# Optimization experiments

Hardware: AMD Instinct MI355X
Metric: run time of the kernel (lower is better)

The kernel has to match this reference:

```python
import jax, jax.numpy as jnp
import numpy as np

NBINS = 256  # skimage threshold_otsu default


def _otsu_threshold(x):
    """Global Otsu threshold over the whole array, matching skimage.filters.threshold_otsu."""
    counts, edges = jnp.histogram(x.reshape(-1), bins=NBINS)
    counts = counts.astype(jnp.float32)
    centers = 0.5 * (edges[:-1] + edges[1:])  # [NBINS]

    # class probabilities / weights for all candidate thresholds
    w1 = jnp.cumsum(counts)                       # weight of class <= t
    w2 = jnp.cumsum(counts[::-1])[::-1]           # weight of class > t
    csum = jnp.cumsum(counts * centers)
    csum_rev = jnp.cumsum((counts * centers)[::-1])[::-1]
    m1 = csum / jnp.maximum(w1, 1.0)              # class means (guard empty bins)
    m2 = csum_rev / jnp.maximum(w2, 1.0)

    # between-class variance at each split point
    var12 = w1[:-1] * w2[1:] * (m1[:-1] - m2[1:]) ** 2  # [NBINS-1]
    idx = jnp.argmax(var12)
    return centers[idx]


def setup_inputs() -> dict:
    key = jax.random.key(0)
    inputs = jax.random.normal(key, (16, 1024, 2048, 1), dtype=jnp.float32)
    return {"inputs": inputs}


def reference(inputs) -> jnp.ndarray:
    x = inputs.astype(jnp.float32)
    thresh = _otsu_threshold(x)
    # ((image > thresh) * 1).astype(float32)
    return (x > thresh).astype(jnp.float32)
```

## Files before the change

### kernel.cpp

```cpp
#include <hip/hip_runtime.h>
#include <stdint.h>

#define NBINS 256
#define NCOPY 32
#define GRID 2048
#define TPB 256
#define HOFF 4
#define MOFF 512
#define XOFF (512 + GRID)
#define PKOFF 8192

typedef float f32x4 __attribute__((ext_vector_type(4)));

__device__ __forceinline__ float edge_at(int i, float minv, float delta) {
    return __fadd_rn(__fmul_rn((float)i, delta), minv);
}
__device__ __forceinline__ float min4(float4 v) {
    return fminf(fminf(v.x, v.y), fminf(v.z, v.w));
}
__device__ __forceinline__ float max4(float4 v) {
    return fmaxf(fmaxf(v.x, v.y), fmaxf(v.z, v.w));
}

__global__ void __launch_bounds__(TPB) k_minmax(const float* __restrict__ in,
                                                int n, uint32_t* ws) {
    float* fws = (float*)ws;
    int n4 = n >> 2;
    int chunk = (n4 + GRID - 1) / GRID;
    int start = blockIdx.x * chunk;
    int end = start + chunk; if (end > n4) end = n4;
    const float4* in4 = (const float4*)in;
    float vmin = INFINITY, vmax = -INFINITY;

    int i = start + threadIdx.x;
    for (; i + 7 * TPB < end; i += 8 * TPB) {
        float4 v0 = in4[i];
        float4 v1 = in4[i + TPB];
        float4 v2 = in4[i + 2 * TPB];
        float4 v3 = in4[i + 3 * TPB];
        float4 v4 = in4[i + 4 * TPB];
        float4 v5 = in4[i + 5 * TPB];
        float4 v6 = in4[i + 6 * TPB];
        float4 v7 = in4[i + 7 * TPB];
        float mn0 = fminf(fminf(min4(v0), min4(v1)), fminf(min4(v2), min4(v3)));
        float mn1 = fminf(fminf(min4(v4), min4(v5)), fminf(min4(v6), min4(v7)));
        float mx0 = fmaxf(fmaxf(max4(v0), max4(v1)), fmaxf(max4(v2), max4(v3)));
        float mx1 = fmaxf(fmaxf(max4(v4), max4(v5)), fmaxf(max4(v6), max4(v7)));
        vmin = fminf(vmin, fminf(mn0, mn1));
        vmax = fmaxf(vmax, fmaxf(mx0, mx1));
    }
    for (; i < end; i += TPB) {
        float4 v = in4[i];
        vmin = fminf(vmin, min4(v));
        vmax = fmaxf(vmax, max4(v));
    }
    for (int j = (n4 << 2) + blockIdx.x * TPB + threadIdx.x; j < n; j += GRID * TPB) {
        float v = in[j];
        vmin = fminf(vmin, v);
        vmax = fmaxf(vmax, v);
    }
#pragma unroll
    for (int off = 32; off > 0; off >>= 1) {
        vmin = fminf(vmin, __shfl_down(vmin, off));
        vmax = fmaxf(vmax, __shfl_down(vmax, off));
    }
    __shared__ float smin[4], smax[4];
    int wave = threadIdx.x >> 6, lane = threadIdx.x & 63;
    if (lane == 0) { smin[wave] = vmin; smax[wave] = vmax; }
    __syncthreads();
    if (threadIdx.x == 0) {
        fws[MOFF + blockIdx.x] = fminf(fminf(smin[0], smin[1]), fminf(smin[2], smin[3]));
        fws[XOFF + blockIdx.x] = fmaxf(fmaxf(smax[0], smax[1]), fmaxf(smax[2], smax[3]));
    }
    if (blockIdx.x == 0) ws[HOFF + threadIdx.x] = 0;
}

__device__ __forceinline__ int bin_of(float v, float minv, float invd) {
    float t = (v - minv) * invd;
    t = fminf(fmaxf(t, 0.0f), 255.0f);
    return (int)t;
}

__device__ __forceinline__ uint32_t binbit(float v, float minv, float invd,
                                           float delta, uint32_t* bit) {
    int j = bin_of(v, minv, invd);
    float e0 = edge_at(j, minv, delta);
    float e1 = edge_at(j + 1, minv, delta);
    float ctr = __fmul_rn(0.5f, __fadd_rn(e0, e1));
    *bit = (v > ctr) ? 1u : 0u;
    return (uint32_t)j;
}

__global__ void __launch_bounds__(TPB) k_hist(const float* __restrict__ in,
                                              int n, uint32_t* ws, int packed) {
    __shared__ uint32_t h[NBINS * NCOPY];
    float* hf = (float*)h;
    float* fws = (float*)ws;

    float lmin = INFINITY, lmax = -INFINITY;
    for (int k = threadIdx.x; k < GRID; k += TPB) {
        lmin = fminf(lmin, fws[MOFF + k]);
        lmax = fmaxf(lmax, fws[XOFF + k]);
    }
#pragma unroll
    for (int off = 32; off > 0; off >>= 1) {
        lmin = fminf(lmin, __shfl_down(lmin, off));
        lmax = fmaxf(lmax, __shfl_down(lmax, off));
    }
    int wave = threadIdx.x >> 6, lane = threadIdx.x & 63;
    if (lane == 0) { hf[wave] = lmin; hf[8 + wave] = lmax; }
    __syncthreads();
    float minv = fminf(fminf(hf[0], hf[1]), fminf(hf[2], hf[3]));
    float maxv = fmaxf(fmaxf(hf[8], hf[9]), fmaxf(hf[10], hf[11]));
    float invd = __fdiv_rn(256.0f, __fsub_rn(maxv, minv));
    float delta = __fdiv_rn(__fsub_rn(maxv, minv), 256.0f);
    __syncthreads();
    for (int i = threadIdx.x; i < NBINS * NCOPY; i += TPB) h[i] = 0;
    __syncthreads();

    int c = threadIdx.x & (NCOPY - 1);
    int n4 = n >> 2;
    int chunk = (n4 + GRID - 1) / GRID;
    int start = blockIdx.x * chunk;
    int end = start + chunk; if (end > n4) end = n4;
    const float4* in4 = (const float4*)in;
    uint32_t* bins = ws + PKOFF;
    uint8_t* bits8 = (uint8_t*)(ws + PKOFF + n4);

    for (int i = start + threadIdx.x; i < end; i += TPB) {
        float4 q = in4[i];
        uint32_t b0, b1, b2, b3;
        uint32_t j0 = binbit(q.x, minv, invd, delta, &b0);
        uint32_t j1 = binbit(q.y, minv, invd, delta, &b1);
        uint32_t j2 = binbit(q.z, minv, invd, delta, &b2);
        uint32_t j3 = binbit(q.w, minv, invd, delta, &b3);
        atomicAdd(&h[j0 * NCOPY + c], 1u);
        atomicAdd(&h[j1 * NCOPY + c], 1u);
        atomicAdd(&h[j2 * NCOPY + c], 1u);
        atomicAdd(&h[j3 * NCOPY + c], 1u);
        if (packed) {
            bins[i] = j0 | (j1 << 8) | (j2 << 16) | (j3 << 24);
            bits8[i] = (uint8_t)(b0 | (b1 << 1) | (b2 << 2) | (b3 << 3));
        }
    }
    for (int j = (n4 << 2) + blockIdx.x * TPB + threadIdx.x; j < n; j += GRID * TPB) {
        atomicAdd(&h[bin_of(in[j], minv, invd) * NCOPY + c], 1u);
    }
    __syncthreads();
    for (int b = threadIdx.x; b < NBINS; b += TPB) {
        uint32_t s = 0;
#pragma unroll
        for (int k = 0; k < NCOPY; ++k) s += h[b * NCOPY + k];
        if (s) atomicAdd(&ws[HOFF + b], s);
    }
}

__device__ __forceinline__ void otsu_prologue(const uint32_t* __restrict__ ws,
                                              int* best_out, float* thresh_out) {
    __shared__ float cnt[NBINS], ctr[NBINS], w1[NBINS], w2[NBINS],
                     cs[NBINS], csr[NBINS], scan[NBINS];
    __shared__ int sbest;
    const float* fws = (const float*)ws;
    int i = threadIdx.x;

    float lmin = INFINITY, lmax = -INFINITY;
    for (int k = i; k < GRID; k += TPB) {
        lmin = fminf(lmin, fws[MOFF + k]);
        lmax = fmaxf(lmax, fws[XOFF + k]);
    }
#pragma unroll
    for (int off = 32; off > 0; off >>= 1) {
        lmin = fminf(lmin, __shfl_down(lmin, off));
        lmax = fmaxf(lmax, __shfl_down(lmax, off));
    }
    int wave = i >> 6, lane = i & 63;
    if (lane == 0) { scan[wave] = lmin; scan[8 + wave] = lmax; }
    __syncthreads();
    float minv = fminf(fminf(scan[0], scan[1]), fminf(scan[2], scan[3]));
    float maxv = fmaxf(fmaxf(scan[8], scan[9]), fmaxf(scan[10], scan[11]));
    float delta = __fdiv_rn(__fsub_rn(maxv, minv), 256.0f);
    __syncthreads();

    cnt[i] = (float)ws[HOFF + i];
    float e0 = edge_at(i, minv, delta);
    float e1 = edge_at(i + 1, minv, delta);
    ctr[i] = __fmul_rn(0.5f, __fadd_rn(e0, e1));
    __syncthreads();

    scan[i] = cnt[i]; __syncthreads();
    for (int off = 1; off < NBINS; off <<= 1) {
        float v = scan[i];
        if (i >= off) v = __fadd_rn(scan[i - off], v);
        __syncthreads(); scan[i] = v; __syncthreads();
    }
    w1[i] = scan[i]; __syncthreads();

    scan[i] = __fmul_rn(cnt[i], ctr[i]); __syncthreads();
    for (int off = 1; off < NBINS; off <<= 1) {
        float v = scan[i];
        if (i >= off) v = __fadd_rn(scan[i - off], v);
        __syncthreads(); scan[i] = v; __syncthreads();
    }
    cs[i] = scan[i]; __syncthreads();

    scan[i] = cnt[i]; __syncthreads();
    for (int off = 1; off < NBINS; off <<= 1) {
        float v = scan[i];
        if (i + off < NBINS) v = __fadd_rn(v, scan[i + off]);
        __syncthreads(); scan[i] = v; __syncthreads();
    }
    w2[i] = scan[i]; __syncthreads();

    scan[i] = __fmul_rn(cnt[i], ctr[i]); __syncthreads();
    for (int off = 1; off < NBINS; off <<= 1) {
        float v = scan[i];
        if (i + off < NBINS) v = __fadd_rn(v, scan[i + off]);
        __syncthreads(); scan[i] = v; __syncthreads();
    }
    csr[i] = scan[i]; __syncthreads();

    if (i < NBINS - 1) {
        float m1 = __fdiv_rn(cs[i], fmaxf(w1[i], 1.0f));
        float m2 = __fdiv_rn(csr[i + 1], fmaxf(w2[i + 1], 1.0f));
        float d = __fsub_rn(m1, m2);
        scan[i] = __fmul_rn(__fmul_rn(w1[i], w2[i + 1]), __fmul_rn(d, d));
    }
    __syncthreads();
    if (i == 0) {
        int best = 0; float bv = scan[0];
        for (int k = 1; k < NBINS - 1; ++k) {
            float v = scan[k];
            if (v > bv) { bv = v; best = k; }
        }
        sbest = best;
        scan[0] = ctr[best];
    }
    __syncthreads();
    *best_out = sbest;
    *thresh_out = scan[0];
    __syncthreads();
}

__device__ __forceinline__ f32x4 verdict4(uint32_t u, uint32_t bt, uint32_t ubest) {
    f32x4 r;
    uint32_t j0 = u & 255u, j1 = (u >> 8) & 255u,
             j2 = (u >> 16) & 255u, j3 = (u >> 24) & 255u;
    r.x = (j0 > ubest || (j0 == ubest && (bt & 1u))) ? 1.0f : 0.0f;
    r.y = (j1 > ubest || (j1 == ubest && (bt & 2u))) ? 1.0f : 0.0f;
    r.z = (j2 > ubest || (j2 == ubest && (bt & 4u))) ? 1.0f : 0.0f;
    r.w = (j3 > ubest || (j3 == ubest && (bt & 8u))) ? 1.0f : 0.0f;
    return r;
}

__global__ void __launch_bounds__(TPB) k_bin_packed(const float* __restrict__ in,
                                                    float* __restrict__ out,
                                                    int n,
                                                    const uint32_t* __restrict__ ws) {
    int best; float t;
    otsu_prologue(ws, &best, &t);

    int n4 = n >> 2;
    int chunk = (n4 + GRID - 1) / GRID;
    int start = blockIdx.x * chunk;
    int end = start + chunk; if (end > n4) end = n4;
    const uint32_t* bins = ws + PKOFF;
    const uint8_t* bits8 = (const uint8_t*)(ws + PKOFF + n4);
    f32x4* out4 = (f32x4*)out;
    uint32_t ubest = (uint32_t)best;

    for (int i = start + threadIdx.x; i < end; i += TPB) {
        f32x4 r = verdict4(bins[i], bits8[i], ubest);
        __builtin_nontemporal_store(r, &out4[i]);
    }
    for (int j = (n4 << 2) + blockIdx.x * TPB + threadIdx.x; j < n; j += GRID * TPB) {
        float r = in[j] > t ? 1.0f : 0.0f;
        __builtin_nontemporal_store(r, &out[j]);
    }
}

__global__ void __launch_bounds__(TPB) k_bin_direct(const float* __restrict__ in,
                                                    float* __restrict__ out,
                                                    int n,
                                                    const uint32_t* __restrict__ ws) {
    int best; float t;
    otsu_prologue(ws, &best, &t);

    int n4 = n >> 2;
    int chunk = (n4 + GRID - 1) / GRID;
    int start = blockIdx.x * chunk;
    int end = start + chunk; if (end > n4) end = n4;
    const float4* in4 = (const float4*)in;
    float4* out4 = (float4*)out;
    int i = start + threadIdx.x;
    for (; i + 3 * TPB < end; i += 4 * TPB) {
        float4 v0 = in4[i];
        float4 v1 = in4[i + TPB];
        float4 v2 = in4[i + 2 * TPB];
        float4 v3 = in4[i + 3 * TPB];
        float4 r0, r1, r2, r3;
        r0.x = v0.x > t ? 1.0f : 0.0f; r0.y = v0.y > t ? 1.0f : 0.0f;
        r0.z = v0.z > t ? 1.0f : 0.0f; r0.w = v0.w > t ? 1.0f : 0.0f;
        r1.x = v1.x > t ? 1.0f : 0.0f; r1.y = v1.y > t ? 1.0f : 0.0f;
        r1.z = v1.z > t ? 1.0f : 0.0f; r1.w = v1.w > t ? 1.0f : 0.0f;
        r2.x = v2.x > t ? 1.0f : 0.0f; r2.y = v2.y > t ? 1.0f : 0.0f;
        r2.z = v2.z > t ? 1.0f : 0.0f; r2.w = v2.w > t ? 1.0f : 0.0f;
        r3.x = v3.x > t ? 1.0f : 0.0f; r3.y = v3.y > t ? 1.0f : 0.0f;
        r3.z = v3.z > t ? 1.0f : 0.0f; r3.w = v3.w > t ? 1.0f : 0.0f;
        out4[i] = r0;
        out4[i + TPB] = r1;
        out4[i + 2 * TPB] = r2;
        out4[i + 3 * TPB] = r3;
    }
    for (; i < end; i += TPB) {
        float4 v = in4[i];
        float4 r;
        r.x = v.x > t ? 1.0f : 0.0f;
        r.y = v.y > t ? 1.0f : 0.0f;
        r.z = v.z > t ? 1.0f : 0.0f;
        r.w = v.w > t ? 1.0f : 0.0f;
        out4[i] = r;
    }
    for (int j = (n4 << 2) + blockIdx.x * TPB + threadIdx.x; j < n; j += GRID * TPB) {
        out[j] = in[j] > t ? 1.0f : 0.0f;
    }
}

extern "C" void kernel_launch(void* const* d_in, const int* in_sizes, int n_in,
                              void* d_out, int out_size, void* d_ws, size_t ws_size,
                              hipStream_t stream) {
    const float* in = (const float*)d_in[0];
    float* out = (float*)d_out;
    uint32_t* ws = (uint32_t*)d_ws;
    int n = in_sizes[0];
    int n4 = n >> 2;

    size_t need = (size_t)(PKOFF + (size_t)n4) * 4 + (size_t)n4;
    int packed = (ws_size >= need) ? 1 : 0;

    hipLaunchKernelGGL(k_minmax, dim3(GRID), dim3(TPB), 0, stream, in, n, ws);
    hipLaunchKernelGGL(k_hist, dim3(GRID), dim3(TPB), 0, stream, in, n, ws, packed);
    if (packed) {
        hipLaunchKernelGGL(k_bin_packed, dim3(GRID), dim3(TPB), 0, stream,
                           in, out, n, ws);
    } else {
        hipLaunchKernelGGL(k_bin_direct, dim3(GRID), dim3(TPB), 0, stream,
                           in, out, n, ws);
    }
}
```

Before: 142.2 us.

## Compute Otsu threshold once in last histogram block via atomic ticket

Moves the Otsu scan/argmax out of every block of the binarize kernels and into the histogram kernel: the last block to finish (detected with an atomic ticket counter) computes the best bin and threshold and publishes them to workspace. The binarize kernels then just read two words instead of each of 2048 blocks re-reducing min/max and running four serial shared-memory scans. The histogram kernel gains a fence and atomic per block, and the tail block does the serial work. It reuses the histogram shared buffer for scan storage and relies on minv/delta already being available there.

```diff
diff --git a/kernel.cpp b/kernel.cpp
--- a/kernel.cpp
+++ b/kernel.cpp
@@ -5,6 +5,9 @@
 #define NCOPY 32
 #define GRID 2048
 #define TPB 256
+#define BEST 1
+#define THRS 2
+#define TICK 3
 #define HOFF 4
 #define MOFF 512
 #define XOFF (512 + GRID)
@@ -72,7 +75,10 @@
         fws[MOFF + blockIdx.x] = fminf(fminf(smin[0], smin[1]), fminf(smin[2], smin[3]));
         fws[XOFF + blockIdx.x] = fmaxf(fmaxf(smax[0], smax[1]), fmaxf(smax[2], smax[3]));
     }
-    if (blockIdx.x == 0) ws[HOFF + threadIdx.x] = 0;
+    if (blockIdx.x == 0) {
+        ws[HOFF + threadIdx.x] = 0;
+        if (threadIdx.x == 0) { ws[BEST] = 0; ws[THRS] = 0; ws[TICK] = 0; }
+    }
 }
 
 __device__ __forceinline__ int bin_of(float v, float minv, float invd) {
@@ -153,92 +159,87 @@
         for (int k = 0; k < NCOPY; ++k) s += h[b * NCOPY + k];
         if (s) atomicAdd(&ws[HOFF + b], s);
     }
-}
-
-__device__ __forceinline__ void otsu_prologue(const uint32_t* __restrict__ ws,
-                                              int* best_out, float* thresh_out) {
-    __shared__ float cnt[NBINS], ctr[NBINS], w1[NBINS], w2[NBINS],
-                     cs[NBINS], csr[NBINS], scan[NBINS];
-    __shared__ int sbest;
-    const float* fws = (const float*)ws;
-    int i = threadIdx.x;
-
-    float lmin = INFINITY, lmax = -INFINITY;
-    for (int k = i; k < GRID; k += TPB) {
-        lmin = fminf(lmin, fws[MOFF + k]);
-        lmax = fmaxf(lmax, fws[XOFF + k]);
-    }
-#pragma unroll
-    for (int off = 32; off > 0; off >>= 1) {
-        lmin = fminf(lmin, __shfl_down(lmin, off));
-        lmax = fmaxf(lmax, __shfl_down(lmax, off));
-    }
-    int wave = i >> 6, lane = i & 63;
-    if (lane == 0) { scan[wave] = lmin; scan[8 + wave] = lmax; }
-    __syncthreads();
-    float minv = fminf(fminf(scan[0], scan[1]), fminf(scan[2], scan[3]));
-    float maxv = fmaxf(fmaxf(scan[8], scan[9]), fmaxf(scan[10], scan[11]));
-    float delta = __fdiv_rn(__fsub_rn(maxv, minv), 256.0f);
-    __syncthreads();
-
-    cnt[i] = (float)ws[HOFF + i];
-    float e0 = edge_at(i, minv, delta);
-    float e1 = edge_at(i + 1, minv, delta);
-    ctr[i] = __fmul_rn(0.5f, __fadd_rn(e0, e1));
-    __syncthreads();
-
-    scan[i] = cnt[i]; __syncthreads();
-    for (int off = 1; off < NBINS; off <<= 1) {
-        float v = scan[i];
-        if (i >= off) v = __fadd_rn(scan[i - off], v);
-        __syncthreads(); scan[i] = v; __syncthreads();
-    }
-    w1[i] = scan[i]; __syncthreads();
-
-    scan[i] = __fmul_rn(cnt[i], ctr[i]); __syncthreads();
-    for (int off = 1; off < NBINS; off <<= 1) {
-        float v = scan[i];
-        if (i >= off) v = __fadd_rn(scan[i - off], v);
-        __syncthreads(); scan[i] = v; __syncthreads();
-    }
-    cs[i] = scan[i]; __syncthreads();
-
-    scan[i] = cnt[i]; __syncthreads();
-    for (int off = 1; off < NBINS; off <<= 1) {
-        float v = scan[i];
-        if (i + off < NBINS) v = __fadd_rn(v, scan[i + off]);
-        __syncthreads(); scan[i] = v; __syncthreads();
-    }
-    w2[i] = scan[i]; __syncthreads();
-
-    scan[i] = __fmul_rn(cnt[i], ctr[i]); __syncthreads();
-    for (int off = 1; off < NBINS; off <<= 1) {
-        float v = scan[i];
-        if (i + off < NBINS) v = __fadd_rn(v, scan[i + off]);
-        __syncthreads(); scan[i] = v; __syncthreads();
-    }
-    csr[i] = scan[i]; __syncthreads();
-
-    if (i < NBINS - 1) {
-        float m1 = __fdiv_rn(cs[i], fmaxf(w1[i], 1.0f));
-        float m2 = __fdiv_rn(csr[i + 1], fmaxf(w2[i + 1], 1.0f));
-        float d = __fsub_rn(m1, m2);
-        scan[i] = __fmul_rn(__fmul_rn(w1[i], w2[i + 1]), __fmul_rn(d, d));
-    }
-    __syncthreads();
-    if (i == 0) {
-        int best = 0; float bv = scan[0];
-        for (int k = 1; k < NBINS - 1; ++k) {
-            float v = scan[k];
-            if (v > bv) { bv = v; best = k; }
-        }
-        sbest = best;
-        scan[0] = ctr[best];
-    }
-    __syncthreads();
-    *best_out = sbest;
-    *thresh_out = scan[0];
-    __syncthreads();
+
+    __syncthreads();
+    __threadfence();
+    if (threadIdx.x == 0) {
+        uint32_t tk = atomicAdd(&ws[TICK], 1u);
+        h[0] = (tk == (uint32_t)(gridDim.x - 1)) ? 1u : 0u;
+    }
+    __syncthreads();
+    if (h[0] == 0) return;
+    __threadfence();
+
+    {
+        float* sf = (float*)h;
+        float* cnt = sf;
+        float* ctr = sf + NBINS;
+        float* w1 = sf + 2 * NBINS;
+        float* w2 = sf + 3 * NBINS;
+        float* cs = sf + 4 * NBINS;
+        float* csr = sf + 5 * NBINS;
+        float* scan = sf + 6 * NBINS;
+        int i = threadIdx.x;
+
+        __syncthreads();
+        cnt[i] = (float)__hip_atomic_load(&ws[HOFF + i], __ATOMIC_RELAXED,
+                                          __HIP_MEMORY_SCOPE_AGENT);
+        float e0 = edge_at(i, minv, delta);
+        float e1 = edge_at(i + 1, minv, delta);
+        ctr[i] = __fmul_rn(0.5f, __fadd_rn(e0, e1));
+        __syncthreads();
+
+        scan[i] = cnt[i]; __syncthreads();
+        for (int off = 1; off < NBINS; off <<= 1) {
+            float v = scan[i];
+            if (i >= off) v = __fadd_rn(scan[i - off], v);
+            __syncthreads(); scan[i] = v; __syncthreads();
+        }
+        w1[i] = scan[i]; __syncthreads();
+
+        scan[i] = __fmul_rn(cnt[i], ctr[i]); __syncthreads();
+        for (int off = 1; off < NBINS; off <<= 1) {
+            float v = scan[i];
+            if (i >= off) v = __fadd_rn(scan[i - off], v);
+            __syncthreads(); scan[i] = v; __syncthreads();
+        }
+        cs[i] = scan[i]; __syncthreads();
+
+        scan[i] = cnt[i]; __syncthreads();
+        for (int off = 1; off < NBINS; off <<= 1) {
+            float v = scan[i];
+            if (i + off < NBINS) v = __fadd_rn(v, scan[i + off]);
+            __syncthreads(); scan[i] = v; __syncthreads();
+        }
+        w2[i] = scan[i]; __syncthreads();
+
+        scan[i] = __fmul_rn(cnt[i], ctr[i]); __syncthreads();
+        for (int off = 1; off < NBINS; off <<= 1) {
+            float v = scan[i];
+            if (i + off < NBINS) v = __fadd_rn(v, scan[i + off]);
+            __syncthreads(); scan[i] = v; __syncthreads();
+        }
+        csr[i] = scan[i]; __syncthreads();
+
+        if (i < NBINS - 1) {
+            float m1 = __fdiv_rn(cs[i], fmaxf(w1[i], 1.0f));
+            float m2 = __fdiv_rn(csr[i + 1], fmaxf(w2[i + 1], 1.0f));
+            float d = __fsub_rn(m1, m2);
+            scan[i] = __fmul_rn(__fmul_rn(w1[i], w2[i + 1]), __fmul_rn(d, d));
+        }
+        __syncthreads();
+        if (i == 0) {
+            int best = 0; float bv = scan[0];
+            for (int k = 1; k < NBINS - 1; ++k) {
+                float v = scan[k];
+                if (v > bv) { bv = v; best = k; }
+            }
+            __hip_atomic_store(&ws[BEST], (uint32_t)best,
+                               __ATOMIC_RELEASE, __HIP_MEMORY_SCOPE_AGENT);
+            __hip_atomic_store(&ws[THRS], __float_as_uint(ctr[best]),
+                               __ATOMIC_RELEASE, __HIP_MEMORY_SCOPE_AGENT);
+        }
+    }
 }
 
 __device__ __forceinline__ f32x4 verdict4(uint32_t u, uint32_t bt, uint32_t ubest) {
@@ -256,8 +257,8 @@
                                                     float* __restrict__ out,
                                                     int n,
                                                     const uint32_t* __restrict__ ws) {
-    int best; float t;
-    otsu_prologue(ws, &best, &t);
+    uint32_t ubest = ws[BEST];
+    float t = __uint_as_float(ws[THRS]);
 
     int n4 = n >> 2;
     int chunk = (n4 + GRID - 1) / GRID;
@@ -266,7 +267,6 @@
     const uint32_t* bins = ws + PKOFF;
     const uint8_t* bits8 = (const uint8_t*)(ws + PKOFF + n4);
     f32x4* out4 = (f32x4*)out;
-    uint32_t ubest = (uint32_t)best;
 
     for (int i = start + threadIdx.x; i < end; i += TPB) {
         f32x4 r = verdict4(bins[i], bits8[i], ubest);
@@ -282,8 +282,7 @@
                                                     float* __restrict__ out,
                                                     int n,
                                                     const uint32_t* __restrict__ ws) {
-    int best; float t;
-    otsu_prologue(ws, &best, &t);
+    float t = __uint_as_float(ws[THRS]);
 
     int n4 = n >> 2;
     int chunk = (n4 + GRID - 1) / GRID;
```

Result: slower. 290.3 us (+104.2%).
